# Kernel optimization log

Measured on AMD Instinct MI355X. Metric: run time of the kernel, lower is better.

Reference implementation:

```python
import jax, jax.numpy as jnp
import numpy as np

HEAD_DIM = 512 // (8 * 2)  # in_dim // (num_heads * 2) = 32
SQRT2 = np.sqrt(2.0).astype(np.float32)


def dwt1d_haar(x):
    # Haar DWT along last dim: L=(even+odd)/sqrt2, H=(even-odd)/sqrt2
    xe, xo = x[..., 0::2], x[..., 1::2]
    return (xe + xo) / SQRT2, (xe - xo) / SQRT2


def idwt1d_haar(L, H):
    # Inverse: even=(L+H)/sqrt2, odd=(L-H)/sqrt2, interleaved
    even = (L + H) / SQRT2
    odd = (L - H) / SQRT2
    x = jnp.stack([even, odd], axis=-1)  # [..., D/2, 2]
    return x.reshape(*x.shape[:-2], -1)  # [..., D]


def setup_inputs() -> dict:
    key = jax.random.key(0)
    k1, k2, k3, k4 = jax.random.split(key, 4)
    B, S, D = 8, 2048, 512
    queries = jax.random.normal(k1, (B, S, D), dtype=jnp.float32)
    keys = jax.random.normal(k2, (B, S, D), dtype=jnp.float32)
    values = jax.random.normal(k3, (B, S, D), dtype=jnp.float32)
    W_o = jax.random.normal(k4, (D, D), dtype=jnp.float32) * (1.0 / np.sqrt(D))
    b_o = jnp.zeros((D,), dtype=jnp.float32)
    return {"queries": queries, "keys": keys, "values": values, "W_o": W_o, "b_o": b_o}


def reference(queries, keys, values, W_o, b_o):
    scale = 1.0 / jnp.sqrt(jnp.asarray(HEAD_DIM, dtype=queries.dtype))
    q_L, q_H = dwt1d_haar(queries)
    k_L, k_H = dwt1d_haar(keys)
    v_L, v_H = dwt1d_haar(values)
    # [B,S,S] score matrices for each wavelet branch
    attn_L = jax.nn.softmax(jnp.einsum("bqd,bkd->bqk", q_L, k_L) * scale, axis=-1)
    attn_H = jax.nn.softmax(jnp.einsum("bqd,bkd->bqk", q_H, k_H) * scale, axis=-1)
    L_out = jnp.einsum("bqk,bkd->bqd", attn_L, v_L)
    H_out = jnp.einsum("bqk,bkd->bqd", attn_H, v_H)
    output = idwt1d_haar(L_out, H_out)  # [B,S,D]
    return output @ W_o.T + b_o
```

## Files before the change

### kernel.cpp

```cpp
#include <hip/hip_runtime.h>

#define INV_SQRT2 0.70710678118654752f
#define QSCALE    0.17677669529663689f

typedef __attribute__((ext_vector_type(8))) short bf16x8;
typedef __attribute__((ext_vector_type(4))) float f32x4;

__device__ __forceinline__ unsigned pack2bf(float a, float b) {
  union { float f; unsigned u; } ua, ub; ua.f = a; ub.f = b;
  unsigned ra = ua.u + 0x7FFFu + ((ua.u >> 16) & 1u);
  unsigned rb = ub.u + 0x7FFFu + ((ub.u >> 16) & 1u);
  return __builtin_amdgcn_perm(rb, ra, 0x07060302);
}

__device__ __forceinline__ void async16(const short* g, short* l) {
  typedef __attribute__((address_space(3))) unsigned lds_u32;
  typedef const __attribute__((address_space(1))) unsigned glb_u32;
  __builtin_amdgcn_global_load_lds((glb_u32*)g, (lds_u32*)l, 16, 0, 0);
}

__global__ void dwt_qk(const float* __restrict__ q, const float* __restrict__ k,
                       short* __restrict__ qs, short* __restrict__ ks) {
  int idx = blockIdx.x * 256 + threadIdx.x;
  int j = idx & 31;
  int s = (idx >> 5) & 2047;
  int b = idx >> 16;
  const float4* qp = (const float4*)(q + ((size_t)(b * 2048 + s)) * 512 + j * 16);
  const float4* kp = (const float4*)(k + ((size_t)(b * 2048 + s)) * 512 + j * 16);
  float4 a0 = qp[0], a1 = qp[1], a2 = qp[2], a3 = qp[3];
  float4 c0 = kp[0], c1 = kp[1], c2 = kp[2], c3 = kp[3];
  union { bf16x8 v; unsigned u[4]; } qL, qH, kL, kH;
  const float cs = INV_SQRT2 * QSCALE;
  qL.u[0] = pack2bf((a0.x + a0.y) * cs, (a0.z + a0.w) * cs);
  qL.u[1] = pack2bf((a1.x + a1.y) * cs, (a1.z + a1.w) * cs);
  qL.u[2] = pack2bf((a2.x + a2.y) * cs, (a2.z + a2.w) * cs);
  qL.u[3] = pack2bf((a3.x + a3.y) * cs, (a3.z + a3.w) * cs);
  qH.u[0] = pack2bf((a0.x - a0.y) * cs, (a0.z - a0.w) * cs);
  qH.u[1] = pack2bf((a1.x - a1.y) * cs, (a1.z - a1.w) * cs);
  qH.u[2] = pack2bf((a2.x - a2.y) * cs, (a2.z - a2.w) * cs);
  qH.u[3] = pack2bf((a3.x - a3.y) * cs, (a3.z - a3.w) * cs);
  kL.u[0] = pack2bf((c0.x + c0.y) * INV_SQRT2, (c0.z + c0.w) * INV_SQRT2);
  kL.u[1] = pack2bf((c1.x + c1.y) * INV_SQRT2, (c1.z + c1.w) * INV_SQRT2);
  kL.u[2] = pack2bf((c2.x + c2.y) * INV_SQRT2, (c2.z + c2.w) * INV_SQRT2);
  kL.u[3] = pack2bf((c3.x + c3.y) * INV_SQRT2, (c3.z + c3.w) * INV_SQRT2);
  kH.u[0] = pack2bf((c0.x - c0.y) * INV_SQRT2, (c0.z - c0.w) * INV_SQRT2);
  kH.u[1] = pack2bf((c1.x - c1.y) * INV_SQRT2, (c1.z - c1.w) * INV_SQRT2);
  kH.u[2] = pack2bf((c2.x - c2.y) * INV_SQRT2, (c2.z - c2.w) * INV_SQRT2);
  kH.u[3] = pack2bf((c3.x - c3.y) * INV_SQRT2, (c3.z - c3.w) * INV_SQRT2);
  size_t oL = ((size_t)(b * 2) * 2048 + s) * 256 + j * 8;
  size_t oH = oL + (size_t)2048 * 256;
  *(bf16x8*)(qs + oL) = qL.v;  *(bf16x8*)(qs + oH) = qH.v;
  *(bf16x8*)(ks + oL) = kL.v;  *(bf16x8*)(ks + oH) = kH.v;
}

__global__ void dwt_v(const float* __restrict__ v, short* __restrict__ vt) {
  __shared__ float tL[64][65];
  __shared__ float tH[64][65];
  int t = threadIdx.x;
  int it = blockIdx.x, st = blockIdx.y, b = blockIdx.z;
#pragma unroll
  for (int rep = 0; rep < 8; rep++) {
    int unit = rep * 256 + t;
    int r = unit >> 5, cp = (unit & 31) * 2;
    float4 vv = *(const float4*)(v + ((size_t)(b * 2048 + st * 64 + r)) * 512 + it * 128 + cp * 2);
    tL[r][cp]     = (vv.x + vv.y) * INV_SQRT2;
    tL[r][cp + 1] = (vv.z + vv.w) * INV_SQRT2;
    tH[r][cp]     = (vv.x - vv.y) * INV_SQRT2;
    tH[r][cp + 1] = (vv.z - vv.w) * INV_SQRT2;
  }
  __syncthreads();
#pragma unroll
  for (int rep = 0; rep < 2; rep++) {
    int unit = rep * 256 + t;
    int i = unit >> 3, cc = unit & 7;
    union { bf16x8 v; unsigned u[4]; } pL, pH;
#pragma unroll
    for (int p = 0; p < 4; p++) {
      pL.u[p] = pack2bf(tL[cc * 8 + p * 2][i], tL[cc * 8 + p * 2 + 1][i]);
      pH.u[p] = pack2bf(tH[cc * 8 + p * 2][i], tH[cc * 8 + p * 2 + 1][i]);
    }
    size_t o = ((size_t)(b * 2) * 256 + it * 64 + i) * 2048 + st * 64 + cc * 8;
    *(bf16x8*)(vt + o) = pL.v;
    *(bf16x8*)(vt + o + (size_t)256 * 2048) = pH.v;
  }
}

__launch_bounds__(256, 2)
__global__ void flash_attn(const short* __restrict__ qs, const short* __restrict__ ks,
                           const short* __restrict__ vt, short* __restrict__ os) {
  __shared__ short lds[36864];
  short* klds = lds;
  short* vlds = lds + 16384;

  int tid = threadIdx.x;
  int w = tid >> 6, L = tid & 63, lo = L & 15, hi = L >> 4;
  int bb = blockIdx.x, qb = blockIdx.y;
  short* plds = lds + 32768 + w * 1024;
  int lo7 = lo & 7;

  bf16x8 qf[8];
  const short* qptr = qs + (((size_t)bb * 2048) + qb * 64 + w * 16 + lo) * 256;
#pragma unroll
  for (int kc = 0; kc < 8; kc++)
    qf[kc] = *(const bf16x8*)(qptr + kc * 32 + hi * 8);

  f32x4 oacc[16];
#pragma unroll
  for (int i = 0; i < 16; i++) oacc[i] = (f32x4){0.f, 0.f, 0.f, 0.f};
  float m_i = -1e30f, l_i = 0.f;

  const short* kbase = ks + ((size_t)bb * 2048) * 256;
  const short* vbase = vt + ((size_t)bb * 256) * 2048;

  int koff[8], voff[8];
#pragma unroll
  for (int rep = 0; rep < 8; rep++) {
    int o = w * 8 + rep;
    int r = 2 * o + (L >> 5);
    int c = (L & 31) ^ (r & 7);
    koff[rep] = r * 256 + c * 8;
    int n = 8 * o + (L >> 3);
    int cv = (L & 7) ^ (n & 7);
    voff[rep] = n * 2048 + cv * 8;
  }

#pragma unroll
  for (int rep = 0; rep < 8; rep++)
    async16(kbase + koff[rep], klds + (w * 8 + rep) * 512);
  __syncthreads();

  for (int kt = 0; kt < 32; kt++) {
    f32x4 sa[4];
#pragma unroll
    for (int ct = 0; ct < 4; ct++) sa[ct] = (f32x4){0.f, 0.f, 0.f, 0.f};
#pragma unroll
    for (int kc = 0; kc < 8; kc++) {
#pragma unroll
      for (int ct = 0; ct < 4; ct++) {
        bf16x8 kb = *(const bf16x8*)(klds + (ct * 16 + lo) * 256 +
                                     ((kc * 4 + hi) ^ lo7) * 8);
        sa[ct] = __builtin_amdgcn_mfma_f32_16x16x32_bf16(kb, qf[kc], sa[ct], 0, 0, 0);
      }
    }

    float vmax = sa[0][0];
#pragma unroll
    for (int ct = 0; ct < 4; ct++)
#pragma unroll
      for (int r = 0; r < 4; r++) vmax = fmaxf(vmax, sa[ct][r]);
    vmax = fmaxf(vmax, __shfl_xor(vmax, 16, 64));
    vmax = fmaxf(vmax, __shfl_xor(vmax, 32, 64));
    float mn = fmaxf(m_i, vmax);
    float al = __expf(m_i - mn);
    m_i = mn;
#pragma unroll
    for (int ct = 0; ct < 4; ct++)
#pragma unroll
      for (int r = 0; r < 4; r++) sa[ct][r] = __expf(sa[ct][r] - mn);
    float rs = 0.f;
#pragma unroll
    for (int ct = 0; ct < 4; ct++)
      rs += (sa[ct][0] + sa[ct][1]) + (sa[ct][2] + sa[ct][3]);
    rs += __shfl_xor(rs, 16, 64);
    rs += __shfl_xor(rs, 32, 64);
    l_i = l_i * al + rs;
#pragma unroll
    for (int mt = 0; mt < 16; mt++)
#pragma unroll
      for (int r = 0; r < 4; r++) oacc[mt][r] *= al;

#pragma unroll
    for (int ct = 0; ct < 4; ct++) {
      uint2 d;
      d.x = pack2bf(sa[ct][0], sa[ct][1]);
      d.y = pack2bf(sa[ct][2], sa[ct][3]);
      *(uint2*)(plds + lo * 64 + ((ct * 2 + (hi >> 1)) ^ lo7) * 8 + (hi & 1) * 4) = d;
    }

    __syncthreads();
#pragma unroll
    for (int rep = 0; rep < 8; rep++)
      async16(vbase + (size_t)kt * 64 + voff[rep], vlds + (w * 8 + rep) * 512);
    __syncthreads();

    if (kt < 31) {
#pragma unroll
      for (int rep = 0; rep < 8; rep++)
        async16(kbase + (size_t)(kt + 1) * 16384 + koff[rep],
                klds + (w * 8 + rep) * 512);
    }

    bf16x8 pf[2];
#pragma unroll
    for (int kc = 0; kc < 2; kc++)
      pf[kc] = *(const bf16x8*)(plds + lo * 64 + ((kc * 4 + hi) ^ lo7) * 8);
#pragma unroll
    for (int mt = 0; mt < 16; mt++)
#pragma unroll
      for (int kc = 0; kc < 2; kc++) {
        bf16x8 vb = *(const bf16x8*)(vlds + (mt * 16 + lo) * 64 +
                                     ((kc * 4 + hi) ^ lo7) * 8);
        oacc[mt] = __builtin_amdgcn_mfma_f32_16x16x32_bf16(vb, pf[kc], oacc[mt], 0, 0, 0);
      }

    __syncthreads();
  }

  float inv = 1.f / l_i;
#pragma unroll
  for (int mt = 0; mt < 16; mt++)
#pragma unroll
    for (int rr = 0; rr < 2; rr++) {
      unsigned d = pack2bf(oacc[mt][rr * 2] * inv, oacc[mt][rr * 2 + 1] * inv);
      *(unsigned*)(lds + (w * 16 + lo) * 264 + mt * 16 + hi * 4 + rr * 2) = d;
    }
  __syncthreads();
  short* obase = os + (((size_t)bb * 2048) + qb * 64) * 256;
#pragma unroll
  for (int rep = 0; rep < 8; rep++) {
    int cid = rep * 256 + tid;
    int row = cid >> 5, c = cid & 31;
    *(bf16x8*)(obase + row * 256 + c * 8) = *(const bf16x8*)(lds + row * 264 + c * 8);
  }
}

__launch_bounds__(256, 2)
__global__ void out_gemm(const short* __restrict__ os, const float* __restrict__ W,
                         const float* __restrict__ bo, float* __restrict__ out) {
  __shared__ short alds[128 * 72];
  __shared__ short blds[128 * 72];
  int tid = threadIdx.x;
  int w = tid >> 6, L = tid & 63, lo = L & 15, hi = L >> 4;
  int wr = w >> 1, wc = w & 1;
  int br = blockIdx.x, bc = blockIdx.y;

  f32x4 acc[4][4];
#pragma unroll
  for (int mt = 0; mt < 4; mt++)
#pragma unroll
    for (int nt = 0; nt < 4; nt++)
      acc[mt][nt] = (f32x4){0.f, 0.f, 0.f, 0.f};

  for (int kt = 0; kt < 8; kt++) {
    __syncthreads();
#pragma unroll
    for (int rep = 0; rep < 4; rep++) {
      int cid = rep * 256 + tid;
      int mrow = cid >> 3, c = cid & 7;
      int gk = kt * 64 + c * 8;
      int half = gk >> 8, i = gk & 255;
      int gr = br * 128 + mrow;
      int b = gr >> 11, s = gr & 2047;
      *(bf16x8*)(alds + mrow * 72 + c * 8) =
          *(const bf16x8*)(os + ((size_t)((b * 2 + half) * 2048 + s)) * 256 + i);
    }
#pragma unroll
    for (int rep = 0; rep < 4; rep++) {
      int cid = rep * 256 + tid;
      int nrow = cid >> 3, c = cid & 7;
      int gk = kt * 64 + c * 8;
      int half = gk >> 8, i = gk & 255;
      const float4* wsrc = (const float4*)(W + (size_t)(bc * 128 + nrow) * 512 + 2 * i);
      float4 f0 = wsrc[0], f1 = wsrc[1], f2 = wsrc[2], f3 = wsrc[3];
      float sg = half ? -INV_SQRT2 : INV_SQRT2;
      union { bf16x8 v; unsigned u[4]; } pk;
      pk.u[0] = pack2bf(f0.x * INV_SQRT2 + f0.y * sg, f0.z * INV_SQRT2 + f0.w * sg);
      pk.u[1] = pack2bf(f1.x * INV_SQRT2 + f1.y * sg, f1.z * INV_SQRT2 + f1.w * sg);
      pk.u[2] = pack2bf(f2.x * INV_SQRT2 + f2.y * sg, f2.z * INV_SQRT2 + f2.w * sg);
      pk.u[3] = pack2bf(f3.x * INV_SQRT2 + f3.y * sg, f3.z * INV_SQRT2 + f3.w * sg);
      *(bf16x8*)(blds + nrow * 72 + c * 8) = pk.v;
    }
    __syncthreads();
    bf16x8 af[4], bfr[4];
#pragma unroll
    for (int kc = 0; kc < 2; kc++) {
#pragma unroll
      for (int mt = 0; mt < 4; mt++)
        af[mt] = *(const bf16x8*)(alds + (wr * 64 + mt * 16 + lo) * 72 + kc * 32 + hi * 8);
#pragma unroll
      for (int nt = 0; nt < 4; nt++)
        bfr[nt] = *(const bf16x8*)(blds + (wc * 64 + nt * 16 + lo) * 72 + kc * 32 + hi * 8);
#pragma unroll
      for (int mt = 0; mt < 4; mt++)
#pragma unroll
        for (int nt = 0; nt < 4; nt++)
          acc[mt][nt] = __builtin_amdgcn_mfma_f32_16x16x32_bf16(af[mt], bfr[nt], acc[mt][nt], 0, 0, 0);
    }
  }

#pragma unroll
  for (int nt = 0; nt < 4; nt++) {
    int cc = bc * 128 + wc * 64 + nt * 16 + lo;
    float bias = bo[cc];
#pragma unroll
    for (int mt = 0; mt < 4; mt++) {
      int rrbase = br * 128 + wr * 64 + mt * 16 + hi * 4;
#pragma unroll
      for (int r = 0; r < 4; r++)
        out[(size_t)(rrbase + r) * 512 + cc] = acc[mt][nt][r] + bias;
    }
  }
}

extern "C" void kernel_launch(void* const* d_in, const int* in_sizes, int n_in,
                              void* d_out, int out_size, void* d_ws, size_t ws_size,
                              hipStream_t stream) {
  const float* q  = (const float*)d_in[0];
  const float* k  = (const float*)d_in[1];
  const float* v  = (const float*)d_in[2];
  const float* W  = (const float*)d_in[3];
  const float* bo = (const float*)d_in[4];
  short* ws  = (short*)d_ws;
  short* qs  = ws;
  short* ksb = ws + (size_t)8  * 1024 * 1024;
  short* vtp = ws + (size_t)16 * 1024 * 1024;
  short* osb = ws + (size_t)24 * 1024 * 1024;

  dwt_qk<<<2048, 256, 0, stream>>>(q, k, qs, ksb);
  dwt_v<<<dim3(4, 32, 8), 256, 0, stream>>>(v, vtp);
  flash_attn<<<dim3(16, 32), 256, 0, stream>>>(qs, ksb, vtp, osb);
  out_gemm<<<dim3(128, 4), 256, 0, stream>>>(osb, W, bo, (float*)d_out);
}
```

Measured before the change: 276.1 us.

## Switch flash attention to 32x32 MFMA with 2x2 wave tiling

Reorganizes the four waves into a 2x2 grid over query rows and key columns and uses 32x32x16 MFMA instead of 16x16x32 for both QK and PV. Each wave computes a 32x32 score tile, so row max and row sum are now exchanged between wave pairs through small LDS buffers, which adds a barrier. The V tile load is issued at the start of the iteration so it overlaps the QK compute, and one barrier is removed. The aim is fewer MFMA issues, less fragment reloading from LDS and better overlap, at the cost of more registers for Q fragments and extra cross-wave sync.

```diff
diff --git a/kernel.cpp b/kernel.cpp
--- a/kernel.cpp
+++ b/kernel.cpp
@@ -5,6 +5,7 @@
 
 typedef __attribute__((ext_vector_type(8))) short bf16x8;
 typedef __attribute__((ext_vector_type(4))) float f32x4;
+typedef __attribute__((ext_vector_type(16))) float f32x16;
 
 __device__ __forceinline__ unsigned pack2bf(float a, float b) {
   union { float f; unsigned u; } ua, ub; ua.f = a; ub.f = b;
@@ -88,25 +89,30 @@
 __launch_bounds__(256, 2)
 __global__ void flash_attn(const short* __restrict__ qs, const short* __restrict__ ks,
                            const short* __restrict__ vt, short* __restrict__ os) {
-  __shared__ short lds[36864];
+  __shared__ short lds[37376];
   short* klds = lds;
   short* vlds = lds + 16384;
+  short* plds = lds + 32768;
+  float* mbuf = (float*)(lds + 36864);
+  float* rbuf = mbuf + 128;
 
   int tid = threadIdx.x;
-  int w = tid >> 6, L = tid & 63, lo = L & 15, hi = L >> 4;
+  int w = tid >> 6, L = tid & 63;
+  int lq = L & 31, hi = L >> 5;
+  int qt = w & 1, ct = w >> 1;
   int bb = blockIdx.x, qb = blockIdx.y;
-  short* plds = lds + 32768 + w * 1024;
-  int lo7 = lo & 7;
-
-  bf16x8 qf[8];
-  const short* qptr = qs + (((size_t)bb * 2048) + qb * 64 + w * 16 + lo) * 256;
-#pragma unroll
-  for (int kc = 0; kc < 8; kc++)
-    qf[kc] = *(const bf16x8*)(qptr + kc * 32 + hi * 8);
-
-  f32x4 oacc[16];
-#pragma unroll
-  for (int i = 0; i < 16; i++) oacc[i] = (f32x4){0.f, 0.f, 0.f, 0.f};
+
+  bf16x8 qf[16];
+  const short* qptr = qs + (((size_t)bb * 2048) + qb * 64 + qt * 32 + lq) * 256 + hi * 8;
+#pragma unroll
+  for (int ksI = 0; ksI < 16; ksI++)
+    qf[ksI] = *(const bf16x8*)(qptr + ksI * 16);
+
+  f32x16 oacc[4];
+#pragma unroll
+  for (int mt = 0; mt < 4; mt++)
+#pragma unroll
+    for (int i = 0; i < 16; i++) oacc[mt][i] = 0.f;
   float m_i = -1e30f, l_i = 0.f;
 
   const short* kbase = ks + ((size_t)bb * 2048) * 256;
@@ -124,95 +130,91 @@
     voff[rep] = n * 2048 + cv * 8;
   }
 
+  int krow = ct * 32 + lq, ksw = krow & 7;
+  int qrow = qt * 32 + lq, qsw = qrow & 7;
+  int mlid = (ct * 2 + qt) * 32 + lq;
+  int mlot = ((ct ^ 1) * 2 + qt) * 32 + lq;
+
 #pragma unroll
   for (int rep = 0; rep < 8; rep++)
     async16(kbase + koff[rep], klds + (w * 8 + rep) * 512);
   __syncthreads();
 
   for (int kt = 0; kt < 32; kt++) {
-    f32x4 sa[4];
-#pragma unroll
-    for (int ct = 0; ct < 4; ct++) sa[ct] = (f32x4){0.f, 0.f, 0.f, 0.f};
-#pragma unroll
-    for (int kc = 0; kc < 8; kc++) {
-#pragma unroll
-      for (int ct = 0; ct < 4; ct++) {
-        bf16x8 kb = *(const bf16x8*)(klds + (ct * 16 + lo) * 256 +
-                                     ((kc * 4 + hi) ^ lo7) * 8);
-        sa[ct] = __builtin_amdgcn_mfma_f32_16x16x32_bf16(kb, qf[kc], sa[ct], 0, 0, 0);
-      }
-    }
-
-    float vmax = sa[0][0];
-#pragma unroll
-    for (int ct = 0; ct < 4; ct++)
-#pragma unroll
-      for (int r = 0; r < 4; r++) vmax = fmaxf(vmax, sa[ct][r]);
-    vmax = fmaxf(vmax, __shfl_xor(vmax, 16, 64));
+#pragma unroll
+    for (int rep = 0; rep < 8; rep++)
+      async16(vbase + (size_t)kt * 64 + voff[rep], vlds + (w * 8 + rep) * 512);
+
+    f32x16 sacc;
+#pragma unroll
+    for (int i = 0; i < 16; i++) sacc[i] = 0.f;
+#pragma unroll
+    for (int ksI = 0; ksI < 16; ksI++) {
+      bf16x8 kb = *(const bf16x8*)(klds + krow * 256 + (((ksI << 1) | hi) ^ ksw) * 8);
+      sacc = __builtin_amdgcn_mfma_f32_32x32x16_bf16(kb, qf[ksI], sacc, 0, 0, 0);
+    }
+
+    float vmax = sacc[0];
+#pragma unroll
+    for (int i = 1; i < 16; i++) vmax = fmaxf(vmax, sacc[i]);
     vmax = fmaxf(vmax, __shfl_xor(vmax, 32, 64));
-    float mn = fmaxf(m_i, vmax);
+    if (hi == 0) mbuf[mlid] = vmax;
+    __syncthreads();
+    float mn = fmaxf(m_i, fmaxf(vmax, mbuf[mlot]));
     float al = __expf(m_i - mn);
     m_i = mn;
 #pragma unroll
-    for (int ct = 0; ct < 4; ct++)
-#pragma unroll
-      for (int r = 0; r < 4; r++) sa[ct][r] = __expf(sa[ct][r] - mn);
+    for (int i = 0; i < 16; i++) sacc[i] = __expf(sacc[i] - mn);
     float rs = 0.f;
 #pragma unroll
-    for (int ct = 0; ct < 4; ct++)
-      rs += (sa[ct][0] + sa[ct][1]) + (sa[ct][2] + sa[ct][3]);
-    rs += __shfl_xor(rs, 16, 64);
+    for (int i = 0; i < 16; i++) rs += sacc[i];
     rs += __shfl_xor(rs, 32, 64);
-    l_i = l_i * al + rs;
-#pragma unroll
-    for (int mt = 0; mt < 16; mt++)
-#pragma unroll
-      for (int r = 0; r < 4; r++) oacc[mt][r] *= al;
-
-#pragma unroll
-    for (int ct = 0; ct < 4; ct++) {
+    if (hi == 0) rbuf[mlid] = rs;
+#pragma unroll
+    for (int g = 0; g < 4; g++) {
       uint2 d;
-      d.x = pack2bf(sa[ct][0], sa[ct][1]);
-      d.y = pack2bf(sa[ct][2], sa[ct][3]);
-      *(uint2*)(plds + lo * 64 + ((ct * 2 + (hi >> 1)) ^ lo7) * 8 + (hi & 1) * 4) = d;
-    }
-
-    __syncthreads();
-#pragma unroll
-    for (int rep = 0; rep < 8; rep++)
-      async16(vbase + (size_t)kt * 64 + voff[rep], vlds + (w * 8 + rep) * 512);
-    __syncthreads();
+      d.x = pack2bf(sacc[4 * g], sacc[4 * g + 1]);
+      d.y = pack2bf(sacc[4 * g + 2], sacc[4 * g + 3]);
+      *(uint2*)(plds + qrow * 64 + ((4 * ct + g) ^ qsw) * 8 + hi * 4) = d;
+    }
+#pragma unroll
+    for (int mt = 0; mt < 4; mt++)
+#pragma unroll
+      for (int i = 0; i < 16; i++) oacc[mt][i] *= al;
+    __syncthreads();
+    l_i = l_i * al + rs + rbuf[mlot];
 
     if (kt < 31) {
 #pragma unroll
       for (int rep = 0; rep < 8; rep++)
-        async16(kbase + (size_t)(kt + 1) * 16384 + koff[rep],
-                klds + (w * 8 + rep) * 512);
-    }
-
-    bf16x8 pf[2];
-#pragma unroll
-    for (int kc = 0; kc < 2; kc++)
-      pf[kc] = *(const bf16x8*)(plds + lo * 64 + ((kc * 4 + hi) ^ lo7) * 8);
-#pragma unroll
-    for (int mt = 0; mt < 16; mt++)
-#pragma unroll
-      for (int kc = 0; kc < 2; kc++) {
-        bf16x8 vb = *(const bf16x8*)(vlds + (mt * 16 + lo) * 64 +
-                                     ((kc * 4 + hi) ^ lo7) * 8);
-        oacc[mt] = __builtin_amdgcn_mfma_f32_16x16x32_bf16(vb, pf[kc], oacc[mt], 0, 0, 0);
+        async16(kbase + (size_t)(kt + 1) * 16384 + koff[rep], klds + (w * 8 + rep) * 512);
+    }
+
+    bf16x8 pb[4];
+#pragma unroll
+    for (int ks4 = 0; ks4 < 4; ks4++)
+      pb[ks4] = *(const bf16x8*)(plds + qrow * 64 + (((ks4 << 1) | hi) ^ qsw) * 8);
+#pragma unroll
+    for (int mt = 0; mt < 4; mt++) {
+      int vrow = ct * 128 + mt * 32 + lq, vsw = vrow & 7;
+#pragma unroll
+      for (int ks4 = 0; ks4 < 4; ks4++) {
+        bf16x8 vb = *(const bf16x8*)(vlds + vrow * 64 + (((ks4 << 1) | hi) ^ vsw) * 8);
+        oacc[mt] = __builtin_amdgcn_mfma_f32_32x32x16_bf16(vb, pb[ks4], oacc[mt], 0, 0, 0);
       }
-
+    }
     __syncthreads();
   }
 
   float inv = 1.f / l_i;
 #pragma unroll
-  for (int mt = 0; mt < 16; mt++)
-#pragma unroll
-    for (int rr = 0; rr < 2; rr++) {
-      unsigned d = pack2bf(oacc[mt][rr * 2] * inv, oacc[mt][rr * 2 + 1] * inv);
-      *(unsigned*)(lds + (w * 16 + lo) * 264 + mt * 16 + hi * 4 + rr * 2) = d;
+  for (int mt = 0; mt < 4; mt++)
+#pragma unroll
+    for (int g = 0; g < 4; g++) {
+      uint2 d;
+      d.x = pack2bf(oacc[mt][4 * g] * inv, oacc[mt][4 * g + 1] * inv);
+      d.y = pack2bf(oacc[mt][4 * g + 2] * inv, oacc[mt][4 * g + 3] * inv);
+      *(uint2*)(lds + qrow * 264 + ct * 128 + mt * 32 + 8 * g + 4 * hi) = d;
     }
   __syncthreads();
   short* obase = os + (((size_t)bb * 2048) + qb * 64) * 256;
```

New measurement: 269.5 us. 1.02x faster.
